# Performance work log

Hardware: AMD Instinct MI355X
Metric: run time of the kernel (lower is better)

The kernel has to match this reference:

```python
import jax, jax.numpy as jnp
import numpy as np

HIDDEN = 1024


def setup_inputs() -> dict:
    key = jax.random.key(0)
    ks = jax.random.split(key, 8)
    x_in, y_in, out_dim, hidden = 1024, 1024, 1024, HIDDEN
    Nx, Ny = 4096, 4096
    s = lambda d: 1.0 / np.sqrt(d)
    return {
        "x": jax.random.normal(ks[0], (Nx, x_in), jnp.float32),
        "y": jax.random.normal(ks[1], (Ny, y_in), jnp.float32),
        "Wq": jax.random.normal(ks[2], (hidden, x_in), jnp.float32) * s(x_in),
        "bq": jnp.zeros((hidden,), jnp.float32),
        "Wk": jax.random.normal(ks[3], (hidden, y_in), jnp.float32) * s(y_in),
        "bk": jnp.zeros((hidden,), jnp.float32),
        "Wv": jax.random.normal(ks[4], (out_dim, y_in), jnp.float32) * s(y_in),
        "bv": jnp.zeros((out_dim,), jnp.float32),
    }


def reference(x, y, Wq, bq, Wk, bk, Wv, bv):
    # Linear projections (torch Linear: x @ W.T + b)
    q = x @ Wq.T + bq          # [Nx, H]
    k = y @ Wk.T + bk          # [Ny, H]
    v = y @ Wv.T + bv          # [Ny, D_out]
    scores = (q @ k.T) / jnp.sqrt(jnp.asarray(HIDDEN, q.dtype))  # [Nx, Ny]
    attn = jax.nn.softmax(scores, axis=1)
    return attn @ v            # [Nx, D_out]
```

## Files before the change

kernel.cpp:

```cpp
#include <hip/hip_runtime.h>
#include <cstdint>
#include <cstddef>

typedef __attribute__((ext_vector_type(8))) __bf16 bf16x8;
typedef __attribute__((ext_vector_type(4))) float  f32x4;

#define WAITCNT_VM(n)   ((n & 0xF) | 0x70 | 0xF00 | (((n) >> 4) << 14))
#define WAITCNT_LGKM(n) (0xF | 0x70 | ((n) << 8) | (3 << 14))

__device__ __forceinline__ unsigned short f32_to_bf16(float f) {
    union { float f; unsigned int u; } cv;
    cv.f = f;
    unsigned int u = cv.u;
    return (unsigned short)((u + 0x7fffu + ((u >> 16) & 1u)) >> 16);
}

__device__ __forceinline__ float bf16_to_f32(unsigned short h) {
    union { unsigned int u; float f; } cv;
    cv.u = ((unsigned int)h) << 16;
    return cv.f;
}

__device__ __forceinline__ void async_copy16(const unsigned short* g, unsigned short* lds) {
    __builtin_amdgcn_global_load_lds(
        (const __attribute__((address_space(1))) unsigned int*)g,
        (__attribute__((address_space(3))) unsigned int*)lds,
        16, 0, 0);
}

__global__ __launch_bounds__(256) void cast_all(
    const float* __restrict__ x,  const float* __restrict__ y,
    const float* __restrict__ wq, const float* __restrict__ wk, const float* __restrict__ wv,
    unsigned short* __restrict__ xb,  unsigned short* __restrict__ yb,
    unsigned short* __restrict__ wqb, unsigned short* __restrict__ wkb,
    unsigned short* __restrict__ wvb, float* __restrict__ lsum)
{
    int b = blockIdx.x;
    if (b >= 11264) {
        float4 z = {0.f, 0.f, 0.f, 0.f};
#pragma unroll
        for (int t = 0; t < 4; ++t)
            ((float4*)lsum)[threadIdx.x * 4 + t] = z;
        return;
    }
    const float* s; unsigned short* d; int base;
    if      (b < 4096)  { s = x;  d = xb;  base = b; }
    else if (b < 8192)  { s = y;  d = yb;  base = b - 4096; }
    else if (b < 9216)  { s = wq; d = wqb; base = b - 8192; }
    else if (b < 10240) { s = wk; d = wkb; base = b - 9216; }
    else                { s = wv; d = wvb; base = b - 10240; }
    int i = base * 256 + threadIdx.x;
    float4 v = ((const float4*)s)[i];
    ushort4 o;
    o.x = f32_to_bf16(v.x);
    o.y = f32_to_bf16(v.y);
    o.z = f32_to_bf16(v.z);
    o.w = f32_to_bf16(v.w);
    ((ushort4*)d)[i] = o;
}

__device__ __forceinline__ void gemm_core_pf(
    const unsigned short* __restrict__ A, const unsigned short* __restrict__ B,
    int K, int rowBase, int colBase, int kBeg, int kEnd,
    unsigned short* ldsA, unsigned short* ldsB, f32x4 acc[4][4])
{
    const int tid  = threadIdx.x;
    const int lane = tid & 63;
    const int wave = tid >> 6;
    const int quad = lane >> 4;
    const int r    = lane & 15;
    const int wm   = wave >> 1;
    const int wn   = wave & 1;

    const int c1 = tid + 256;
    const long aOff0 = (long)(rowBase + (tid >> 2)) * K + (tid & 3) * 8;
    const long aOff1 = (long)(rowBase + (c1  >> 2)) * K + (c1  & 3) * 8;
    const long bOff0 = (long)(colBase + (tid >> 2)) * K + (tid & 3) * 8;
    const long bOff1 = (long)(colBase + (c1  >> 2)) * K + (c1  & 3) * 8;
    unsigned short* ldsA0 = ldsA + tid * 8;
    unsigned short* ldsA1 = ldsA + c1 * 8;
    unsigned short* ldsB0 = ldsB + tid * 8;
    unsigned short* ldsB1 = ldsB + c1 * 8;

    const int aReadOff = (wm * 64 + r) * 32 + quad * 8;
    const int bReadOff = (wn * 64 + r) * 32 + quad * 8;

    const int nSteps = (kEnd - kBeg) >> 5;

    async_copy16(A + aOff0 + kBeg, ldsA0);
    async_copy16(A + aOff1 + kBeg, ldsA1);
    async_copy16(B + bOff0 + kBeg, ldsB0);
    async_copy16(B + bOff1 + kBeg, ldsB1);

    for (int s = 0; s < nSteps; ++s) {
        const int cur = (s & 1) << 12;
        const int nxt = cur ^ 4096;
        __builtin_amdgcn_s_waitcnt(0);
        __syncthreads();
        if (s + 1 < nSteps) {
            const int kn = kBeg + ((s + 1) << 5);
            async_copy16(A + aOff0 + kn, ldsA0 + nxt);
            async_copy16(A + aOff1 + kn, ldsA1 + nxt);
            async_copy16(B + bOff0 + kn, ldsB0 + nxt);
            async_copy16(B + bOff1 + kn, ldsB1 + nxt);
        }
        bf16x8 af[4], bfr[4];
#pragma unroll
        for (int i = 0; i < 4; ++i)
            af[i] = *(const bf16x8*)(ldsA + cur + aReadOff + i * 16 * 32);
#pragma unroll
        for (int j = 0; j < 4; ++j)
            bfr[j] = *(const bf16x8*)(ldsB + cur + bReadOff + j * 16 * 32);
#pragma unroll
        for (int i = 0; i < 4; ++i)
#pragma unroll
            for (int j = 0; j < 4; ++j)
                acc[i][j] = __builtin_amdgcn_mfma_f32_16x16x32_bf16(af[i], bfr[j], acc[i][j], 0, 0, 0);
    }
}

__global__ __launch_bounds__(256, 2)
void proj_batched(const unsigned short* __restrict__ xb, const unsigned short* __restrict__ yb,
                  const unsigned short* __restrict__ wqb, const unsigned short* __restrict__ wkb,
                  const unsigned short* __restrict__ wvb,
                  unsigned short* __restrict__ q, unsigned short* __restrict__ k,
                  unsigned short* __restrict__ vt,
                  const float* __restrict__ bq, const float* __restrict__ bk,
                  const float* __restrict__ bv)
{
    __shared__ __align__(16) unsigned short ldsA[2 * 128 * 32];
    __shared__ __align__(16) unsigned short ldsB[2 * 128 * 32];

    const int b = blockIdx.x;
    const int z = b >> 8;
    const int rb = b & 255;

    const unsigned short *A, *B;
    unsigned short* C;
    const float* bias;
    int N, rowBase, colBase;
    bool biasPerRow;
    if (z == 0) {
        A = xb; B = wqb; C = q; bias = bq; N = 1024; biasPerRow = false;
        colBase = (rb >> 5) * 128; rowBase = (rb & 31) * 128;
    } else if (z == 1) {
        A = yb; B = wkb; C = k; bias = bk; N = 1024; biasPerRow = false;
        colBase = (rb >> 5) * 128; rowBase = (rb & 31) * 128;
    } else {
        A = wvb; B = yb; C = vt; bias = bv; N = 4096; biasPerRow = true;
        colBase = (rb >> 3) * 128; rowBase = (rb & 7) * 128;
    }

    f32x4 acc[4][4];
#pragma unroll
    for (int i = 0; i < 4; ++i)
#pragma unroll
        for (int j = 0; j < 4; ++j)
            acc[i][j] = (f32x4){0.f, 0.f, 0.f, 0.f};

    gemm_core_pf(A, B, 1024, rowBase, colBase, 0, 1024, ldsA, ldsB, acc);

    const int lane = threadIdx.x & 63;
    const int wave = threadIdx.x >> 6;
    const int quad = lane >> 4;
    const int r    = lane & 15;
    const int orow0 = rowBase + (wave >> 1) * 64 + quad * 4;
    const int ocol0 = colBase + (wave & 1) * 64 + r;

#pragma unroll
    for (int i = 0; i < 4; ++i)
#pragma unroll
        for (int e = 0; e < 4; ++e) {
            const int row = orow0 + i * 16 + e;
            const float brow = biasPerRow ? bias[row] : 0.f;
#pragma unroll
            for (int j = 0; j < 4; ++j) {
                const int col = ocol0 + j * 16;
                const float bb = biasPerRow ? brow : bias[col];
                C[(long)row * N + col] = f32_to_bf16(acc[i][j][e] + bb);
            }
        }
}

__device__ __forceinline__ void stage_half(const unsigned short* src, long rstep,
                                           unsigned short* ldsLane) {
    async_copy16(src, ldsLane);
    async_copy16(src + rstep, ldsLane + 4096);
}

__device__ __forceinline__ void gemm256_core(
    const unsigned short* __restrict__ A, const unsigned short* __restrict__ B,
    int K, int rowBase, int colBase, int kBeg, int nTiles,
    unsigned short* lds, f32x4 acc[8][4])
{
    const int tid  = threadIdx.x;
    const int lane = tid & 63;
    const int wid  = tid >> 6;
    const int quad = lane >> 4;
    const int r    = lane & 15;
    const int wm   = wid >> 2;
    const int wn   = wid & 3;

    const int row0 = tid >> 3;
    const int chs8 = (((tid & 7) ^ (row0 & 7)) << 3);
    const unsigned short* As = A + (long)(rowBase + row0) * K + chs8 + kBeg;
    const unsigned short* Bs = B + (long)(colBase + row0) * K + chs8 + kBeg;
    const long rstep = (long)K * 64;
    const long hstep = (long)K * 128;
    unsigned short* ldsLane = lds + tid * 8;

    const int aRd = (wm << 13) + (r << 6);
    const int bRd = 16384 + (wn << 12) + (r << 6);
    const int sw0 = ((quad ^ (r & 7)) << 3);
    const int sw1 = (((quad + 4) ^ (r & 7)) << 3);

    stage_half(As,         rstep, ldsLane);
    stage_half(As + hstep, rstep, ldsLane + 8192);
    stage_half(Bs,         rstep, ldsLane + 16384);
    stage_half(Bs + hstep, rstep, ldsLane + 24576);
    if (nTiles > 1) {
        stage_half(Bs + 64,         rstep, ldsLane + 32768 + 16384);
        stage_half(Bs + hstep + 64, rstep, ldsLane + 32768 + 24576);
    }
    __builtin_amdgcn_s_waitcnt(WAITCNT_VM(4));
    __builtin_amdgcn_s_barrier();
    __builtin_amdgcn_sched_barrier(0);

    bf16x8 aE[4], aO[4], bX[4], bY[4];
#pragma unroll
    for (int i = 0; i < 4; ++i)
        aE[i] = *(const bf16x8*)(lds + aRd + i * 1024 + sw0);
#pragma unroll
    for (int j = 0; j < 4; ++j)
        bX[j] = *(const bf16x8*)(lds + bRd + j * 1024 + sw0);

    for (int T = 0; T < nTiles; ++T) {
        const int cur = (T & 1) << 15;
        const int nxt = cur ^ 32768;

#pragma unroll
        for (int i = 0; i < 4; ++i)
            aO[i] = *(const bf16x8*)(lds + cur + aRd + (4 + i) * 1024 + sw0);
        __builtin_amdgcn_s_waitcnt(WAITCNT_LGKM(4));
        __builtin_amdgcn_sched_barrier(0);
        __builtin_amdgcn_s_setprio(1);
#pragma unroll
        for (int i = 0; i < 4; ++i)
#pragma unroll
            for (int j = 0; j < 4; ++j)
                acc[i][j] = __builtin_amdgcn_mfma_f32_16x16x32_bf16(aE[i], bX[j], acc[i][j], 0, 0, 0);
        __builtin_amdgcn_s_setprio(0);
        __builtin_amdgcn_sched_barrier(0);
        __builtin_amdgcn_s_barrier();
        if (T + 1 < nTiles) stage_half(As + (T + 1) * 64, rstep, ldsLane + nxt);

#pragma unroll
        for (int i = 0; i < 4; ++i)
            aE[i] = *(const bf16x8*)(lds + cur + aRd + i * 1024 + sw1);
#pragma unroll
        for (int j = 0; j < 4; ++j)
            bY[j] = *(const bf16x8*)(lds + cur + bRd + j * 1024 + sw1);
        __builtin_amdgcn_s_waitcnt(WAITCNT_LGKM(8));
        __builtin_amdgcn_sched_barrier(0);
        __builtin_amdgcn_s_setprio(1);
#pragma unroll
        for (int i = 0; i < 4; ++i)
#pragma unroll
            for (int j = 0; j < 4; ++j)
                acc[4 + i][j] = __builtin_amdgcn_mfma_f32_16x16x32_bf16(aO[i], bX[j], acc[4 + i][j], 0, 0, 0);
        __builtin_amdgcn_s_setprio(0);
        __builtin_amdgcn_sched_barrier(0);
        __builtin_amdgcn_s_barrier();
        if (T + 1 < nTiles) stage_half(As + hstep + (T + 1) * 64, rstep, ldsLane + nxt + 8192);

#pragma unroll
        for (int i = 0; i < 4; ++i)
            aO[i] = *(const bf16x8*)(lds + cur + aRd + (4 + i) * 1024 + sw1);
        __builtin_amdgcn_s_waitcnt(WAITCNT_LGKM(4));
        __builtin_amdgcn_sched_barrier(0);
        __builtin_amdgcn_s_setprio(1);
#pragma unroll
        for (int i = 0; i < 4; ++i)
#pragma unroll
            for (int j = 0; j < 4; ++j)
                acc[i][j] = __builtin_amdgcn_mfma_f32_16x16x32_bf16(aE[i], bY[j], acc[i][j], 0, 0, 0);
        __builtin_amdgcn_s_setprio(0);
        __builtin_amdgcn_sched_barrier(0);
        __builtin_amdgcn_s_barrier();
        if (T + 2 < nTiles) stage_half(Bs + (T + 2) * 64, rstep, ldsLane + cur + 16384);

        if (T + 1 < nTiles) {
            if (T + 2 < nTiles) __builtin_amdgcn_s_waitcnt(WAITCNT_VM(2));
            else                __builtin_amdgcn_s_waitcnt(WAITCNT_VM(0));
            __builtin_amdgcn_s_barrier();
            __builtin_amdgcn_sched_barrier(0);
#pragma unroll
            for (int i = 0; i < 4; ++i)
                aE[i] = *(const bf16x8*)(lds + nxt + aRd + i * 1024 + sw0);
#pragma unroll
            for (int j = 0; j < 4; ++j)
                bX[j] = *(const bf16x8*)(lds + nxt + bRd + j * 1024 + sw0);
            __builtin_amdgcn_s_waitcnt(WAITCNT_LGKM(8));
        } else {
            __builtin_amdgcn_s_waitcnt(WAITCNT_LGKM(0));
        }
        __builtin_amdgcn_sched_barrier(0);
        __builtin_amdgcn_s_setprio(1);
#pragma unroll
        for (int i = 0; i < 4; ++i)
#pragma unroll
            for (int j = 0; j < 4; ++j)
                acc[4 + i][j] = __builtin_amdgcn_mfma_f32_16x16x32_bf16(aO[i], bY[j], acc[4 + i][j], 0, 0, 0);
        __builtin_amdgcn_s_setprio(0);
        __builtin_amdgcn_sched_barrier(0);
        if (T + 2 < nTiles) stage_half(Bs + hstep + (T + 2) * 64, rstep, ldsLane + cur + 24576);
    }
}

__global__ __launch_bounds__(512, 2)
void scores_gemm256(const unsigned short* __restrict__ q, const unsigned short* __restrict__ k,
                    unsigned short* __restrict__ P, float* __restrict__ lsum, float scale2)
{
    __shared__ __align__(16) unsigned short lds[2 * 32768];

    const int bid = blockIdx.x;
    const int swz = (bid & 7) * 32 + (bid >> 3);
    const int mt = swz >> 4, nt = swz & 15;
    const int rowBase = mt * 256;
    const int colBase = nt * 256;

    f32x4 acc[8][4];
#pragma unroll
    for (int i = 0; i < 8; ++i)
#pragma unroll
        for (int j = 0; j < 4; ++j)
            acc[i][j] = (f32x4){0.f, 0.f, 0.f, 0.f};

    gemm256_core(q, k, 1024, rowBase, colBase, 0, 16, lds, acc);

    const int lane = threadIdx.x & 63;
    const int wid  = threadIdx.x >> 6;
    const int quad = lane >> 4;
    const int r    = lane & 15;
    const int orow0 = rowBase + (wid >> 2) * 128 + quad * 4;
    const int ocol0 = colBase + (wid & 3) * 64 + r;

#pragma unroll
    for (int mi = 0; mi < 8; ++mi)
#pragma unroll
        for (int e = 0; e < 4; ++e) {
            const int row = orow0 + mi * 16 + e;
            float rs = 0.f;
#pragma unroll
            for (int nj = 0; nj < 4; ++nj) {
                const float p = exp2f(acc[mi][nj][e] * scale2);
                rs += p;
                P[(long)row * 4096 + ocol0 + nj * 16] = f32_to_bf16(p);
            }
#pragma unroll
            for (int m = 1; m < 16; m <<= 1) rs += __shfl_xor(rs, m, 64);
            if (r == 0) atomicAdd(&lsum[row], rs);
        }
}

template <int ATOMIC>
__global__ __launch_bounds__(512, 2)
void out_gemm256(const unsigned short* __restrict__ P, const unsigned short* __restrict__ vt,
                 void* __restrict__ Out)
{
    __shared__ __align__(16) unsigned short lds[2 * 32768];

    const int bid = blockIdx.x;
    const int swz = (bid & 7) * 32 + (bid >> 3);
    const int z  = swz & 3;
    const int nt = (swz >> 2) & 3;
    const int mt = swz >> 4;
    const int rowBase = mt * 256;
    const int colBase = nt * 256;
    const int kBeg = z * 1024;

    f32x4 acc[8][4];
#pragma unroll
    for (int i = 0; i < 8; ++i)
#pragma unroll
        for (int j = 0; j < 4; ++j)
            acc[i][j] = (f32x4){0.f, 0.f, 0.f, 0.f};

    gemm256_core(P, vt, 4096, rowBase, colBase, kBeg, 16, lds, acc);

    const int lane = threadIdx.x & 63;
    const int wid  = threadIdx.x >> 6;
    const int quad = lane >> 4;
    const int r    = lane & 15;
    const int orow0 = rowBase + (wid >> 2) * 128 + quad * 4;
    const int ocol0 = colBase + (wid & 3) * 64 + r;

#pragma unroll
    for (int mi = 0; mi < 8; ++mi)
#pragma unroll
        for (int e = 0; e < 4; ++e) {
            const int row = orow0 + mi * 16 + e;
#pragma unroll
            for (int nj = 0; nj < 4; ++nj) {
                const int col = ocol0 + nj * 16;
                if (ATOMIC) {
                    atomicAdd(&((float*)Out)[(long)row * 1024 + col], acc[mi][nj][e]);
                } else {
                    unsigned short* parts = (unsigned short*)Out + (size_t)z * (4096 * 1024);
                    parts[(long)row * 1024 + col] = f32_to_bf16(acc[mi][nj][e]);
                }
            }
        }
}

__global__ __launch_bounds__(256) void reduce_norm4(const unsigned short* __restrict__ parts,
                                                    const float* __restrict__ lsum,
                                                    float* __restrict__ O) {
    const int i = blockIdx.x * 256 + threadIdx.x;
    const float inv = 1.0f / lsum[i >> 8];
    const size_t stride = (size_t)(4096 * 1024) / 4;
    ushort4 a = ((const ushort4*)parts)[i];
    ushort4 b = ((const ushort4*)parts)[i + stride];
    ushort4 c = ((const ushort4*)parts)[i + 2 * stride];
    ushort4 d = ((const ushort4*)parts)[i + 3 * stride];
    float4 o;
    o.x = (bf16_to_f32(a.x) + bf16_to_f32(b.x) + bf16_to_f32(c.x) + bf16_to_f32(d.x)) * inv;
    o.y = (bf16_to_f32(a.y) + bf16_to_f32(b.y) + bf16_to_f32(c.y) + bf16_to_f32(d.y)) * inv;
    o.z = (bf16_to_f32(a.z) + bf16_to_f32(b.z) + bf16_to_f32(c.z) + bf16_to_f32(d.z)) * inv;
    o.w = (bf16_to_f32(a.w) + bf16_to_f32(b.w) + bf16_to_f32(c.w) + bf16_to_f32(d.w)) * inv;
    ((float4*)O)[i] = o;
}

__global__ __launch_bounds__(256) void norm_rows(float* __restrict__ O, const float* __restrict__ lsum) {
    int i = blockIdx.x * 256 + threadIdx.x;
    const float inv = 1.0f / lsum[i >> 8];
    float4 v = ((const float4*)O)[i];
    v.x *= inv; v.y *= inv; v.z *= inv; v.w *= inv;
    ((float4*)O)[i] = v;
}

extern "C" void kernel_launch(void* const* d_in, const int* in_sizes, int n_in,
                              void* d_out, int out_size, void* d_ws, size_t ws_size,
                              hipStream_t stream) {
    const float* x  = (const float*)d_in[0];
    const float* y  = (const float*)d_in[1];
    const float* Wq = (const float*)d_in[2];
    const float* bq = (const float*)d_in[3];
    const float* Wk = (const float*)d_in[4];
    const float* bk = (const float*)d_in[5];
    const float* Wv = (const float*)d_in[6];
    const float* bv = (const float*)d_in[7];

    constexpr int Nx = 4096, Ny = 4096, H = 1024, Dv = 1024, Kin = 1024;

    char* ws = (char*)d_ws;
    size_t off = 0;
    auto carve = [&](size_t bytes) {
        char* p = ws + off;
        off += (bytes + 255) & ~(size_t)255;
        return p;
    };

    unsigned short* q_bf  = (unsigned short*)carve((size_t)Nx * H * 2);
    unsigned short* k_bf  = (unsigned short*)carve((size_t)Ny * H * 2);
    unsigned short* vt_bf = (unsigned short*)carve((size_t)Dv * Ny * 2);
    float*          lsum  = (float*)carve((size_t)Nx * sizeof(float));

    char* overlay = ws + off;
    unsigned short* x_bf  = (unsigned short*)overlay;
    unsigned short* y_bf  = x_bf  + (size_t)Nx * Kin;
    unsigned short* Wq_bf = y_bf  + (size_t)Ny * Kin;
    unsigned short* Wk_bf = Wq_bf + (size_t)H  * Kin;
    unsigned short* Wv_bf = Wk_bf + (size_t)H  * Kin;
    unsigned short* P_bf  = (unsigned short*)overlay;

    const size_t overlay_bytes = (size_t)Nx * Ny * 2;
    const size_t partsBytes = (size_t)Nx * Dv * 2;
    unsigned short* parts = (unsigned short*)(overlay + overlay_bytes);
    const size_t need_parts = (size_t)((overlay + overlay_bytes + 4 * partsBytes) - ws);
    const bool useParts = ws_size >= need_parts;

    if (!useParts)
        hipMemsetAsync(d_out, 0, (size_t)Nx * Dv * sizeof(float), stream);

    cast_all<<<11265, 256, 0, stream>>>(x, y, Wq, Wk, Wv, x_bf, y_bf, Wq_bf, Wk_bf, Wv_bf, lsum);

    proj_batched<<<768, 256, 0, stream>>>(x_bf, y_bf, Wq_bf, Wk_bf, Wv_bf,
                                          q_bf, k_bf, vt_bf, bq, bk, bv);

    const float scale2 = 1.4426950408889634f / 32.0f;
    scores_gemm256<<<256, 512, 0, stream>>>(q_bf, k_bf, P_bf, lsum, scale2);

    if (useParts) {
        out_gemm256<0><<<256, 512, 0, stream>>>(P_bf, vt_bf, parts);
        reduce_norm4<<<(Nx * Dv / 4) / 256, 256, 0, stream>>>(parts, lsum, (float*)d_out);
    } else {
        out_gemm256<1><<<256, 512, 0, stream>>>(P_bf, vt_bf, d_out);
        norm_rows<<<Nx * Dv / 4 / 256, 256, 0, stream>>>((float*)d_out, lsum);
    }
}
```

Baseline: 223.1 us.

## Fuse all attention stages into one cooperative persistent kernel with grid syncs

Replaces the five separate launches (cast, projection, scores, output GEMM, reduce) with a single cooperative kernel of 256 blocks that runs each stage in turn, separated by grid-wide syncs. It also moves the projection GEMM onto the 256x256 latency-tuned GEMM core, so only 192 blocks are active in that stage. The aim is to remove launch gaps and tail effects between kernels. In exchange, the cast and reduce stages run as grid-stride loops on fewer threads, the projection stage leaves some blocks idle, and grid syncs add overhead.

```diff
diff --git a/kernel.cpp b/kernel.cpp
--- a/kernel.cpp
+++ b/kernel.cpp
@@ -1,6 +1,9 @@
 #include <hip/hip_runtime.h>
+#include <hip/hip_cooperative_groups.h>
 #include <cstdint>
 #include <cstddef>
+
+namespace cg = cooperative_groups;
 
 typedef __attribute__((ext_vector_type(8))) __bf16 bf16x8;
 typedef __attribute__((ext_vector_type(4))) float  f32x4;
@@ -26,6 +29,324 @@
         (const __attribute__((address_space(1))) unsigned int*)g,
         (__attribute__((address_space(3))) unsigned int*)lds,
         16, 0, 0);
+}
+
+#define G256_BAR  __builtin_amdgcn_s_barrier()
+#define G256_SB   __builtin_amdgcn_sched_barrier(0)
+#define G256_PR1  __builtin_amdgcn_s_setprio(1)
+#define G256_PR0  __builtin_amdgcn_s_setprio(0)
+
+__device__ __forceinline__ void gemm256_la(
+    const unsigned short* __restrict__ A, const unsigned short* __restrict__ B,
+    int K, int rowBase, int colBase, int kBeg, int nTiles,
+    unsigned short* lds, f32x4 acc[8][4])
+{
+    const int tid  = threadIdx.x;
+    const int lane = tid & 63;
+    const int wid  = tid >> 6;
+    const int quad = lane >> 4;
+    const int r    = lane & 15;
+    const int wm   = wid >> 2;
+    const int wn   = wid & 3;
+
+    const int row0 = tid >> 3;
+    const int chs8 = (((tid & 7) ^ (row0 & 7)) << 3);
+    const unsigned short* As = A + (long)(rowBase + row0) * K + chs8 + kBeg;
+    const unsigned short* Bs = B + (long)(colBase + row0) * K + chs8 + kBeg;
+    const long rstep = (long)K * 64;
+    const long hstep = (long)K * 128;
+    unsigned short* ldsLane = lds + tid * 8;
+
+    const int aRd = (wm << 13) + (r << 6);
+    const int bRd = 16384 + (wn << 12) + (r << 6);
+    const int sw0 = ((quad ^ (r & 7)) << 3);
+    const int sw1 = (((quad + 4) ^ (r & 7)) << 3);
+
+    auto STG = [&](const unsigned short* src, int ldsOff) {
+        async_copy16(src,         ldsLane + ldsOff);
+        async_copy16(src + rstep, ldsLane + ldsOff + 4096);
+    };
+
+    STG(As,         0);
+    STG(As + hstep, 8192);
+    STG(Bs,         16384);
+    STG(Bs + hstep, 24576);
+    if (nTiles > 1) {
+        STG(Bs + 64,         32768 + 16384);
+        STG(Bs + hstep + 64, 32768 + 24576);
+    }
+    __builtin_amdgcn_s_waitcnt(WAITCNT_VM(4));
+    G256_BAR;
+    G256_SB;
+
+    bf16x8 aE[4], aO[4], bX[4], bY[4];
+#pragma unroll
+    for (int i = 0; i < 4; ++i)
+        aE[i] = *(const bf16x8*)(lds + aRd + i * 1024 + sw0);
+#pragma unroll
+    for (int j = 0; j < 4; ++j)
+        bX[j] = *(const bf16x8*)(lds + bRd + j * 1024 + sw0);
+
+    for (int T = 0; T < nTiles; ++T) {
+        const int cur = (T & 1) << 15;
+        const int nxt = cur ^ 32768;
+
+#pragma unroll
+        for (int i = 0; i < 4; ++i)
+            aO[i] = *(const bf16x8*)(lds + cur + aRd + (4 + i) * 1024 + sw0);
+        __builtin_amdgcn_s_waitcnt(WAITCNT_LGKM(4));
+        G256_SB;
+        G256_PR1;
+#pragma unroll
+        for (int i = 0; i < 4; ++i)
+#pragma unroll
+            for (int j = 0; j < 4; ++j)
+                acc[i][j] = __builtin_amdgcn_mfma_f32_16x16x32_bf16(aE[i], bX[j], acc[i][j], 0, 0, 0);
+        G256_PR0;
+        G256_SB;
+        G256_BAR;
+        if (T + 1 < nTiles) STG(As + (T + 1) * 64, nxt);
+
+#pragma unroll
+        for (int i = 0; i < 4; ++i)
+            aE[i] = *(const bf16x8*)(lds + cur + aRd + i * 1024 + sw1);
+#pragma unroll
+        for (int j = 0; j < 4; ++j)
+            bY[j] = *(const bf16x8*)(lds + cur + bRd + j * 1024 + sw1);
+        __builtin_amdgcn_s_waitcnt(WAITCNT_LGKM(8));
+        G256_SB;
+        G256_PR1;
+#pragma unroll
+        for (int i = 0; i < 4; ++i)
+#pragma unroll
+            for (int j = 0; j < 4; ++j)
+                acc[4 + i][j] = __builtin_amdgcn_mfma_f32_16x16x32_bf16(aO[i], bX[j], acc[4 + i][j], 0, 0, 0);
+        G256_PR0;
+        G256_SB;
+        G256_BAR;
+        if (T + 1 < nTiles) STG(As + hstep + (T + 1) * 64, nxt + 8192);
+
+#pragma unroll
+        for (int i = 0; i < 4; ++i)
+            aO[i] = *(const bf16x8*)(lds + cur + aRd + (4 + i) * 1024 + sw1);
+        __builtin_amdgcn_s_waitcnt(WAITCNT_LGKM(4));
+        G256_SB;
+        G256_PR1;
+#pragma unroll
+        for (int i = 0; i < 4; ++i)
+#pragma unroll
+            for (int j = 0; j < 4; ++j)
+                acc[i][j] = __builtin_amdgcn_mfma_f32_16x16x32_bf16(aE[i], bY[j], acc[i][j], 0, 0, 0);
+        G256_PR0;
+        G256_SB;
+        G256_BAR;
+        if (T + 2 < nTiles) STG(Bs + (T + 2) * 64, cur + 16384);
+
+        if (T + 1 < nTiles) {
+            if (T + 2 < nTiles) __builtin_amdgcn_s_waitcnt(WAITCNT_VM(2));
+            else                __builtin_amdgcn_s_waitcnt(WAITCNT_VM(0));
+            G256_BAR;
+            G256_SB;
+#pragma unroll
+            for (int i = 0; i < 4; ++i)
+                aE[i] = *(const bf16x8*)(lds + nxt + aRd + i * 1024 + sw0);
+#pragma unroll
+            for (int j = 0; j < 4; ++j)
+                bX[j] = *(const bf16x8*)(lds + nxt + bRd + j * 1024 + sw0);
+            __builtin_amdgcn_s_waitcnt(WAITCNT_LGKM(8));
+        } else {
+            __builtin_amdgcn_s_waitcnt(WAITCNT_LGKM(0));
+        }
+        G256_SB;
+        G256_PR1;
+#pragma unroll
+        for (int i = 0; i < 4; ++i)
+#pragma unroll
+            for (int j = 0; j < 4; ++j)
+                acc[4 + i][j] = __builtin_amdgcn_mfma_f32_16x16x32_bf16(aO[i], bY[j], acc[4 + i][j], 0, 0, 0);
+        G256_PR0;
+        G256_SB;
+        if (T + 2 < nTiles) STG(Bs + hstep + (T + 2) * 64, cur + 24576);
+    }
+}
+
+__global__ __launch_bounds__(512, 2)
+void mega(const float* __restrict__ x,  const float* __restrict__ y,
+          const float* __restrict__ wq, const float* __restrict__ wk, const float* __restrict__ wv,
+          const float* __restrict__ bq, const float* __restrict__ bk, const float* __restrict__ bv,
+          unsigned short* __restrict__ xb,  unsigned short* __restrict__ yb,
+          unsigned short* __restrict__ wqb, unsigned short* __restrict__ wkb,
+          unsigned short* __restrict__ wvb,
+          unsigned short* __restrict__ q, unsigned short* __restrict__ k,
+          unsigned short* __restrict__ vt, unsigned short* __restrict__ P,
+          unsigned short* __restrict__ parts, float* __restrict__ lsum,
+          float* __restrict__ O, float scale2)
+{
+    __shared__ __align__(16) unsigned short lds[2 * 32768];
+    cg::grid_group gg = cg::this_grid();
+
+    const int tid  = threadIdx.x;
+    const int bid  = blockIdx.x;
+    const long gtid = (long)bid * 512 + tid;
+
+    {
+        float4 z4 = {0.f, 0.f, 0.f, 0.f};
+        for (long u = gtid; u < 2884608L; u += 131072L) {
+            if (u < 1024) { ((float4*)lsum)[u] = z4; continue; }
+            long v = u - 1024;
+            const float* s; unsigned short* d; long idx;
+            if      (v < 1048576L) { s = x;  d = xb;  idx = v; }
+            else if (v < 2097152L) { s = y;  d = yb;  idx = v - 1048576L; }
+            else if (v < 2359296L) { s = wq; d = wqb; idx = v - 2097152L; }
+            else if (v < 2621440L) { s = wk; d = wkb; idx = v - 2359296L; }
+            else                   { s = wv; d = wvb; idx = v - 2621440L; }
+            float4 vv = ((const float4*)s)[idx];
+            ushort4 o;
+            o.x = f32_to_bf16(vv.x);
+            o.y = f32_to_bf16(vv.y);
+            o.z = f32_to_bf16(vv.z);
+            o.w = f32_to_bf16(vv.w);
+            ((ushort4*)d)[idx] = o;
+        }
+    }
+    gg.sync();
+
+    const int lane = tid & 63;
+    const int wid  = tid >> 6;
+    const int quad = lane >> 4;
+    const int rr   = lane & 15;
+
+    if (bid < 192) {
+        const int z  = bid >> 6;
+        const int rb = bid & 63;
+        const unsigned short *A, *B;
+        unsigned short* C;
+        const float* bias;
+        int Nout, rowBase, colBase;
+        bool perRow;
+        if (z == 0) {
+            A = xb; B = wqb; C = q; bias = bq; Nout = 1024; perRow = false;
+            rowBase = (rb >> 2) * 256; colBase = (rb & 3) * 256;
+        } else if (z == 1) {
+            A = yb; B = wkb; C = k; bias = bk; Nout = 1024; perRow = false;
+            rowBase = (rb >> 2) * 256; colBase = (rb & 3) * 256;
+        } else {
+            A = wvb; B = yb; C = vt; bias = bv; Nout = 4096; perRow = true;
+            rowBase = (rb >> 4) * 256; colBase = (rb & 15) * 256;
+        }
+
+        f32x4 acc[8][4];
+#pragma unroll
+        for (int i = 0; i < 8; ++i)
+#pragma unroll
+            for (int j = 0; j < 4; ++j)
+                acc[i][j] = (f32x4){0.f, 0.f, 0.f, 0.f};
+
+        gemm256_la(A, B, 1024, rowBase, colBase, 0, 16, lds, acc);
+
+        const int orow0 = rowBase + (wid >> 2) * 128 + quad * 4;
+        const int ocol0 = colBase + (wid & 3) * 64 + rr;
+#pragma unroll
+        for (int mi = 0; mi < 8; ++mi)
+#pragma unroll
+            for (int e = 0; e < 4; ++e) {
+                const int row = orow0 + mi * 16 + e;
+                const float brow = perRow ? bias[row] : 0.f;
+#pragma unroll
+                for (int nj = 0; nj < 4; ++nj) {
+                    const int col = ocol0 + nj * 16;
+                    const float bb = perRow ? brow : bias[col];
+                    C[(long)row * Nout + col] = f32_to_bf16(acc[mi][nj][e] + bb);
+                }
+            }
+    }
+    gg.sync();
+
+    {
+        const int swz = (bid & 7) * 32 + (bid >> 3);
+        const int mt = swz >> 4, nt = swz & 15;
+        const int rowBase = mt * 256;
+        const int colBase = nt * 256;
+
+        f32x4 acc[8][4];
+#pragma unroll
+        for (int i = 0; i < 8; ++i)
+#pragma unroll
+            for (int j = 0; j < 4; ++j)
+                acc[i][j] = (f32x4){0.f, 0.f, 0.f, 0.f};
+
+        gemm256_la(q, k, 1024, rowBase, colBase, 0, 16, lds, acc);
+
+        const int orow0 = rowBase + (wid >> 2) * 128 + quad * 4;
+        const int ocol0 = colBase + (wid & 3) * 64 + rr;
+#pragma unroll
+        for (int mi = 0; mi < 8; ++mi)
+#pragma unroll
+            for (int e = 0; e < 4; ++e) {
+                const int row = orow0 + mi * 16 + e;
+                float rs = 0.f;
+#pragma unroll
+                for (int nj = 0; nj < 4; ++nj) {
+                    const float p = exp2f(acc[mi][nj][e] * scale2);
+                    rs += p;
+                    P[(long)row * 4096 + ocol0 + nj * 16] = f32_to_bf16(p);
+                }
+#pragma unroll
+                for (int m = 1; m < 16; m <<= 1) rs += __shfl_xor(rs, m, 64);
+                if (rr == 0) atomicAdd(&lsum[row], rs);
+            }
+    }
+    gg.sync();
+
+    {
+        const int swz = (bid & 7) * 32 + (bid >> 3);
+        const int z  = swz & 3;
+        const int nt = (swz >> 2) & 3;
+        const int mt = swz >> 4;
+        const int rowBase = mt * 256;
+        const int colBase = nt * 256;
+        const int kBeg = z * 1024;
+
+        f32x4 acc[8][4];
+#pragma unroll
+        for (int i = 0; i < 8; ++i)
+#pragma unroll
+            for (int j = 0; j < 4; ++j)
+                acc[i][j] = (f32x4){0.f, 0.f, 0.f, 0.f};
+
+        gemm256_la(P, vt, 4096, rowBase, colBase, kBeg, 16, lds, acc);
+
+        unsigned short* part = parts + (size_t)z * (4096 * 1024);
+        const int orow0 = rowBase + (wid >> 2) * 128 + quad * 4;
+        const int ocol0 = colBase + (wid & 3) * 64 + rr;
+#pragma unroll
+        for (int mi = 0; mi < 8; ++mi)
+#pragma unroll
+            for (int e = 0; e < 4; ++e) {
+                const int row = orow0 + mi * 16 + e;
+#pragma unroll
+                for (int nj = 0; nj < 4; ++nj)
+                    part[(long)row * 1024 + ocol0 + nj * 16] = f32_to_bf16(acc[mi][nj][e]);
+            }
+    }
+    gg.sync();
+
+    {
+        const size_t stride = 1048576;
+        for (long i = gtid; i < 1048576L; i += 131072L) {
+            const float inv = 1.0f / lsum[i >> 8];
+            ushort4 a = ((const ushort4*)parts)[i];
+            ushort4 b = ((const ushort4*)parts)[i + stride];
+            ushort4 c = ((const ushort4*)parts)[i + 2 * stride];
+            ushort4 d = ((const ushort4*)parts)[i + 3 * stride];
+            float4 o;
+            o.x = (bf16_to_f32(a.x) + bf16_to_f32(b.x) + bf16_to_f32(c.x) + bf16_to_f32(d.x)) * inv;
+            o.y = (bf16_to_f32(a.y) + bf16_to_f32(b.y) + bf16_to_f32(c.y) + bf16_to_f32(d.y)) * inv;
+            o.z = (bf16_to_f32(a.z) + bf16_to_f32(b.z) + bf16_to_f32(c.z) + bf16_to_f32(d.z)) * inv;
+            o.w = (bf16_to_f32(a.w) + bf16_to_f32(b.w) + bf16_to_f32(c.w) + bf16_to_f32(d.w)) * inv;
+            ((float4*)O)[i] = o;
+        }
+    }
 }
 
 __global__ __launch_bounds__(256) void cast_all(
@@ -59,262 +380,58 @@
     ((ushort4*)d)[i] = o;
 }
 
-__device__ __forceinline__ void gemm_core_pf(
-    const unsigned short* __restrict__ A, const unsigned short* __restrict__ B,
-    int K, int rowBase, int colBase, int kBeg, int kEnd,
-    unsigned short* ldsA, unsigned short* ldsB, f32x4 acc[4][4])
+__global__ __launch_bounds__(512, 2)
+void proj256(const unsigned short* __restrict__ xb, const unsigned short* __restrict__ yb,
+             const unsigned short* __restrict__ wqb, const unsigned short* __restrict__ wkb,
+             const unsigned short* __restrict__ wvb,
+             unsigned short* __restrict__ q, unsigned short* __restrict__ k,
+             unsigned short* __restrict__ vt,
+             const float* __restrict__ bq, const float* __restrict__ bk,
+             const float* __restrict__ bv)
 {
-    const int tid  = threadIdx.x;
-    const int lane = tid & 63;
-    const int wave = tid >> 6;
-    const int quad = lane >> 4;
-    const int r    = lane & 15;
-    const int wm   = wave >> 1;
-    const int wn   = wave & 1;
-
-    const int c1 = tid + 256;
-    const long aOff0 = (long)(rowBase + (tid >> 2)) * K + (tid & 3) * 8;
-    const long aOff1 = (long)(rowBase + (c1  >> 2)) * K + (c1  & 3) * 8;
-    const long bOff0 = (long)(colBase + (tid >> 2)) * K + (tid & 3) * 8;
-    const long bOff1 = (long)(colBase + (c1  >> 2)) * K + (c1  & 3) * 8;
-    unsigned short* ldsA0 = ldsA + tid * 8;
-    unsigned short* ldsA1 = ldsA + c1 * 8;
-    unsigned short* ldsB0 = ldsB + tid * 8;
-    unsigned short* ldsB1 = ldsB + c1 * 8;
-
-    const int aReadOff = (wm * 64 + r) * 32 + quad * 8;
-    const int bReadOff = (wn * 64 + r) * 32 + quad * 8;
-
-    const int nSteps = (kEnd - kBeg) >> 5;
-
-    async_copy16(A + aOff0 + kBeg, ldsA0);
-    async_copy16(A + aOff1 + kBeg, ldsA1);
-    async_copy16(B + bOff0 + kBeg, ldsB0);
-    async_copy16(B + bOff1 + kBeg, ldsB1);
-
-    for (int s = 0; s < nSteps; ++s) {
-        const int cur = (s & 1) << 12;
-        const int nxt = cur ^ 4096;
-        __builtin_amdgcn_s_waitcnt(0);
-        __syncthreads();
-        if (s + 1 < nSteps) {
-            const int kn = kBeg + ((s + 1) << 5);
-            async_copy16(A + aOff0 + kn, ldsA0 + nxt);
-            async_copy16(A + aOff1 + kn, ldsA1 + nxt);
-            async_copy16(B + bOff0 + kn, ldsB0 + nxt);
-            async_copy16(B + bOff1 + kn, ldsB1 + nxt);
-        }
-        bf16x8 af[4], bfr[4];
-#pragma unroll
-        for (int i = 0; i < 4; ++i)
-            af[i] = *(const bf16x8*)(ldsA + cur + aReadOff + i * 16 * 32);
-#pragma unroll
-        for (int j = 0; j < 4; ++j)
-            bfr[j] = *(const bf16x8*)(ldsB + cur + bReadOff + j * 16 * 32);
-#pragma unroll
-        for (int i = 0; i < 4; ++i)
-#pragma unroll
-            for (int j = 0; j < 4; ++j)
-                acc[i][j] = __builtin_amdgcn_mfma_f32_16x16x32_bf16(af[i], bfr[j], acc[i][j], 0, 0, 0);
-    }
-}
-
-__global__ __launch_bounds__(256, 2)
-void proj_batched(const unsigned short* __restrict__ xb, const unsigned short* __restrict__ yb,
-                  const unsigned short* __restrict__ wqb, const unsigned short* __restrict__ wkb,
-                  const unsigned short* __restrict__ wvb,
-                  unsigned short* __restrict__ q, unsigned short* __restrict__ k,
-                  unsigned short* __restrict__ vt,
-                  const float* __restrict__ bq, const float* __restrict__ bk,
-                  const float* __restrict__ bv)
-{
-    __shared__ __align__(16) unsigned short ldsA[2 * 128 * 32];
-    __shared__ __align__(16) unsigned short ldsB[2 * 128 * 32];
-
-    const int b = blockIdx.x;
-    const int z = b >> 8;
-    const int rb = b & 255;
-
+    __shared__ __align__(16) unsigned short lds[2 * 32768];
+    const int bid = blockIdx.x;
+    const int z  = bid >> 6;
+    const int rb = bid & 63;
     const unsigned short *A, *B;
     unsigned short* C;
     const float* bias;
-    int N, rowBase, colBase;
-    bool biasPerRow;
+    int Nout, rowBase, colBase;
+    bool perRow;
     if (z == 0) {
-        A = xb; B = wqb; C = q; bias = bq; N = 1024; biasPerRow = false;
-        colBase = (rb >> 5) * 128; rowBase = (rb & 31) * 128;
+        A = xb; B = wqb; C = q; bias = bq; Nout = 1024; perRow = false;
+        rowBase = (rb >> 2) * 256; colBase = (rb & 3) * 256;
     } else if (z == 1) {
-        A = yb; B = wkb; C = k; bias = bk; N = 1024; biasPerRow = false;
-        colBase = (rb >> 5) * 128; rowBase = (rb & 31) * 128;
+        A = yb; B = wkb; C = k; bias = bk; Nout = 1024; perRow = false;
+        rowBase = (rb >> 2) * 256; colBase = (rb & 3) * 256;
     } else {
-        A = wvb; B = yb; C = vt; bias = bv; N = 4096; biasPerRow = true;
-        colBase = (rb >> 3) * 128; rowBase = (rb & 7) * 128;
-    }
-
-    f32x4 acc[4][4];
-#pragma unroll
-    for (int i = 0; i < 4; ++i)
+        A = wvb; B = yb; C = vt; bias = bv; Nout = 4096; perRow = true;
+        rowBase = (rb >> 4) * 256; colBase = (rb & 15) * 256;
+    }
+    f32x4 acc[8][4];
+#pragma unroll
+    for (int i = 0; i < 8; ++i)
 #pragma unroll
         for (int j = 0; j < 4; ++j)
             acc[i][j] = (f32x4){0.f, 0.f, 0.f, 0.f};
-
-    gemm_core_pf(A, B, 1024, rowBase, colBase, 0, 1024, ldsA, ldsB, acc);
-
+    gemm256_la(A, B, 1024, rowBase, colBase, 0, 16, lds, acc);
     const int lane = threadIdx.x & 63;
-    const int wave = threadIdx.x >> 6;
-    const int quad = lane >> 4;
-    const int r    = lane & 15;
-    const int orow0 = rowBase + (wave >> 1) * 64 + quad * 4;
-    const int ocol0 = colBase + (wave & 1) * 64 + r;
-
-#pragma unroll
-    for (int i = 0; i < 4; ++i)
+    const int wid  = threadIdx.x >> 6;
+    const int orow0 = rowBase + (wid >> 2) * 128 + (lane >> 4) * 4;
+    const int ocol0 = colBase + (wid & 3) * 64 + (lane & 15);
+#pragma unroll
+    for (int mi = 0; mi < 8; ++mi)
 #pragma unroll
         for (int e = 0; e < 4; ++e) {
-            const int row = orow0 + i * 16 + e;
-            const float brow = biasPerRow ? bias[row] : 0.f;
-#pragma unroll
-            for (int j = 0; j < 4; ++j) {
-                const int col = ocol0 + j * 16;
-                const float bb = biasPerRow ? brow : bias[col];
-                C[(long)row * N + col] = f32_to_bf16(acc[i][j][e] + bb);
+            const int row = orow0 + mi * 16 + e;
+            const float brow = perRow ? bias[row] : 0.f;
+#pragma unroll
+            for (int nj = 0; nj < 4; ++nj) {
+                const int col = ocol0 + nj * 16;
+                const float bb = perRow ? brow : bias[col];
+                C[(long)row * Nout + col] = f32_to_bf16(acc[mi][nj][e] + bb);
             }
         }
-}
-
-__device__ __forceinline__ void stage_half(const unsigned short* src, long rstep,
-                                           unsigned short* ldsLane) {
-    async_copy16(src, ldsLane);
-    async_copy16(src + rstep, ldsLane + 4096);
-}
-
-__device__ __forceinline__ void gemm256_core(
-    const unsigned short* __restrict__ A, const unsigned short* __restrict__ B,
-    int K, int rowBase, int colBase, int kBeg, int nTiles,
-    unsigned short* lds, f32x4 acc[8][4])
-{
-    const int tid  = threadIdx.x;
-    const int lane = tid & 63;
-    const int wid  = tid >> 6;
-    const int quad = lane >> 4;
-    const int r    = lane & 15;
-    const int wm   = wid >> 2;
-    const int wn   = wid & 3;
-
-    const int row0 = tid >> 3;
-    const int chs8 = (((tid & 7) ^ (row0 & 7)) << 3);
-    const unsigned short* As = A + (long)(rowBase + row0) * K + chs8 + kBeg;
-    const unsigned short* Bs = B + (long)(colBase + row0) * K + chs8 + kBeg;
-    const long rstep = (long)K * 64;
-    const long hstep = (long)K * 128;
-    unsigned short* ldsLane = lds + tid * 8;
-
-    const int aRd = (wm << 13) + (r << 6);
-    const int bRd = 16384 + (wn << 12) + (r << 6);
-    const int sw0 = ((quad ^ (r & 7)) << 3);
-    const int sw1 = (((quad + 4) ^ (r & 7)) << 3);
-
-    stage_half(As,         rstep, ldsLane);
-    stage_half(As + hstep, rstep, ldsLane + 8192);
-    stage_half(Bs,         rstep, ldsLane + 16384);
-    stage_half(Bs + hstep, rstep, ldsLane + 24576);
-    if (nTiles > 1) {
-        stage_half(Bs + 64,         rstep, ldsLane + 32768 + 16384);
-        stage_half(Bs + hstep + 64, rstep, ldsLane + 32768 + 24576);
-    }
-    __builtin_amdgcn_s_waitcnt(WAITCNT_VM(4));
-    __builtin_amdgcn_s_barrier();
-    __builtin_amdgcn_sched_barrier(0);
-
-    bf16x8 aE[4], aO[4], bX[4], bY[4];
-#pragma unroll
-    for (int i = 0; i < 4; ++i)
-        aE[i] = *(const bf16x8*)(lds + aRd + i * 1024 + sw0);
-#pragma unroll
-    for (int j = 0; j < 4; ++j)
-        bX[j] = *(const bf16x8*)(lds + bRd + j * 1024 + sw0);
-
-    for (int T = 0; T < nTiles; ++T) {
-        const int cur = (T & 1) << 15;
-        const int nxt = cur ^ 32768;
-
-#pragma unroll
-        for (int i = 0; i < 4; ++i)
-            aO[i] = *(const bf16x8*)(lds + cur + aRd + (4 + i) * 1024 + sw0);
-        __builtin_amdgcn_s_waitcnt(WAITCNT_LGKM(4));
-        __builtin_amdgcn_sched_barrier(0);
-        __builtin_amdgcn_s_setprio(1);
-#pragma unroll
-        for (int i = 0; i < 4; ++i)
-#pragma unroll
-            for (int j = 0; j < 4; ++j)
-                acc[i][j] = __builtin_amdgcn_mfma_f32_16x16x32_bf16(aE[i], bX[j], acc[i][j], 0, 0, 0);
-        __builtin_amdgcn_s_setprio(0);
-        __builtin_amdgcn_sched_barrier(0);
-        __builtin_amdgcn_s_barrier();
-        if (T + 1 < nTiles) stage_half(As + (T + 1) * 64, rstep, ldsLane + nxt);
-
-#pragma unroll
-        for (int i = 0; i < 4; ++i)
-            aE[i] = *(const bf16x8*)(lds + cur + aRd + i * 1024 + sw1);
-#pragma unroll
-        for (int j = 0; j < 4; ++j)
-            bY[j] = *(const bf16x8*)(lds + cur + bRd + j * 1024 + sw1);
-        __builtin_amdgcn_s_waitcnt(WAITCNT_LGKM(8));
-        __builtin_amdgcn_sched_barrier(0);
-        __builtin_amdgcn_s_setprio(1);
-#pragma unroll
-        for (int i = 0; i < 4; ++i)
-#pragma unroll
-            for (int j = 0; j < 4; ++j)
-                acc[4 + i][j] = __builtin_amdgcn_mfma_f32_16x16x32_bf16(aO[i], bX[j], acc[4 + i][j], 0, 0, 0);
-        __builtin_amdgcn_s_setprio(0);
-        __builtin_amdgcn_sched_barrier(0);
-        __builtin_amdgcn_s_barrier();
-        if (T + 1 < nTiles) stage_half(As + hstep + (T + 1) * 64, rstep, ldsLane + nxt + 8192);
-
-#pragma unroll
-        for (int i = 0; i < 4; ++i)
-            aO[i] = *(const bf16x8*)(lds + cur + aRd + (4 + i) * 1024 + sw1);
-        __builtin_amdgcn_s_waitcnt(WAITCNT_LGKM(4));
-        __builtin_amdgcn_sched_barrier(0);
-        __builtin_amdgcn_s_setprio(1);
-#pragma unroll
-        for (int i = 0; i < 4; ++i)
-#pragma unroll
-            for (int j = 0; j < 4; ++j)
-                acc[i][j] = __builtin_amdgcn_mfma_f32_16x16x32_bf16(aE[i], bY[j], acc[i][j], 0, 0, 0);
-        __builtin_amdgcn_s_setprio(0);
-        __builtin_amdgcn_sched_barrier(0);
-        __builtin_amdgcn_s_barrier();
-        if (T + 2 < nTiles) stage_half(Bs + (T + 2) * 64, rstep, ldsLane + cur + 16384);
-
-        if (T + 1 < nTiles) {
-            if (T + 2 < nTiles) __builtin_amdgcn_s_waitcnt(WAITCNT_VM(2));
-            else                __builtin_amdgcn_s_waitcnt(WAITCNT_VM(0));
-            __builtin_amdgcn_s_barrier();
-            __builtin_amdgcn_sched_barrier(0);
-#pragma unroll
-            for (int i = 0; i < 4; ++i)
-                aE[i] = *(const bf16x8*)(lds + nxt + aRd + i * 1024 + sw0);
-#pragma unroll
-            for (int j = 0; j < 4; ++j)
-                bX[j] = *(const bf16x8*)(lds + nxt + bRd + j * 1024 + sw0);
-            __builtin_amdgcn_s_waitcnt(WAITCNT_LGKM(8));
-        } else {
-            __builtin_amdgcn_s_waitcnt(WAITCNT_LGKM(0));
-        }
-        __builtin_amdgcn_sched_barrier(0);
-        __builtin_amdgcn_s_setprio(1);
-#pragma unroll
-        for (int i = 0; i < 4; ++i)
-#pragma unroll
-            for (int j = 0; j < 4; ++j)
-                acc[4 + i][j] = __builtin_amdgcn_mfma_f32_16x16x32_bf16(aO[i], bY[j], acc[4 + i][j], 0, 0, 0);
-        __builtin_amdgcn_s_setprio(0);
-        __builtin_amdgcn_sched_barrier(0);
-        if (T + 2 < nTiles) stage_half(Bs + hstep + (T + 2) * 64, rstep, ldsLane + cur + 24576);
-    }
 }
 
 __global__ __launch_bounds__(512, 2)
@@ -322,29 +439,22 @@
                     unsigned short* __restrict__ P, float* __restrict__ lsum, float scale2)
 {
     __shared__ __align__(16) unsigned short lds[2 * 32768];
-
     const int bid = blockIdx.x;
     const int swz = (bid & 7) * 32 + (bid >> 3);
     const int mt = swz >> 4, nt = swz & 15;
     const int rowBase = mt * 256;
     const int colBase = nt * 256;
-
     f32x4 acc[8][4];
 #pragma unroll
     for (int i = 0; i < 8; ++i)
 #pragma unroll
         for (int j = 0; j < 4; ++j)
             acc[i][j] = (f32x4){0.f, 0.f, 0.f, 0.f};
-
-    gemm256_core(q, k, 1024, rowBase, colBase, 0, 16, lds, acc);
-
+    gemm256_la(q, k, 1024, rowBase, colBase, 0, 16, lds, acc);
     const int lane = threadIdx.x & 63;
     const int wid  = threadIdx.x >> 6;
-    const int quad = lane >> 4;
-    const int r    = lane & 15;
-    const int orow0 = rowBase + (wid >> 2) * 128 + quad * 4;
-    const int ocol0 = colBase + (wid & 3) * 64 + r;
-
+    const int orow0 = rowBase + (wid >> 2) * 128 + (lane >> 4) * 4;
+    const int ocol0 = colBase + (wid & 3) * 64 + (lane & 15);
 #pragma unroll
     for (int mi = 0; mi < 8; ++mi)
 #pragma unroll
@@ -359,17 +469,15 @@
             }
 #pragma unroll
             for (int m = 1; m < 16; m <<= 1) rs += __shfl_xor(rs, m, 64);
-            if (r == 0) atomicAdd(&lsum[row], rs);
-        }
-}
-
-template <int ATOMIC>
+            if ((lane & 15) == 0) atomicAdd(&lsum[row], rs);
+        }
+}
+
 __global__ __launch_bounds__(512, 2)
-void out_gemm256(const unsigned short* __restrict__ P, const unsigned short* __restrict__ vt,
-                 void* __restrict__ Out)
+void out_gemm256_atomic(const unsigned short* __restrict__ P, const unsigned short* __restrict__ vt,
+                        float* __restrict__ Out)
 {
     __shared__ __align__(16) unsigned short lds[2 * 32768];
-
     const int bid = blockIdx.x;
     const int swz = (bid & 7) * 32 + (bid >> 3);
     const int z  = swz & 3;
@@ -377,58 +485,26 @@
     const int mt = swz >> 4;
     const int rowBase = mt * 256;
     const int colBase = nt * 256;
-    const int kBeg = z * 1024;
-
     f32x4 acc[8][4];
 #pragma unroll
     for (int i = 0; i < 8; ++i)
 #pragma unroll
         for (int j = 0; j < 4; ++j)
             acc[i][j] = (f32x4){0.f, 0.f, 0.f, 0.f};
-
-    gemm256_core(P, vt, 4096, rowBase, colBase, kBeg, 16, lds, acc);
-
+    gemm256_la(P, vt, 4096, rowBase, colBase, z * 1024, 16, lds, acc);
     const int lane = threadIdx.x & 63;
     const int wid  = threadIdx.x >> 6;
-    const int quad = lane >> 4;
-    const int r    = lane & 15;
-    const int orow0 = rowBase + (wid >> 2) * 128 + quad * 4;
-    const int ocol0 = colBase + (wid & 3) * 64 + r;
-
+    const int orow0 = rowBase + (wid >> 2) * 128 + (lane >> 4) * 4;
+    const int ocol0 = colBase + (wid & 3) * 64 + (lane & 15);
 #pragma unroll
     for (int mi = 0; mi < 8; ++mi)
 #pragma unroll
         for (int e = 0; e < 4; ++e) {
             const int row = orow0 + mi * 16 + e;
 #pragma unroll
-            for (int nj = 0; nj < 4; ++nj) {
-                const int col = ocol0 + nj * 16;
-                if (ATOMIC) {
-                    atomicAdd(&((float*)Out)[(long)row * 1024 + col], acc[mi][nj][e]);
-                } else {
-                    unsigned short* parts = (unsigned short*)Out + (size_t)z * (4096 * 1024);
-                    parts[(long)row * 1024 + col] = f32_to_bf16(acc[mi][nj][e]);
-                }
-            }
-        }
-}
-
-__global__ __launch_bounds__(256) void reduce_norm4(const unsigned short* __restrict__ parts,
-                                                    const float* __restrict__ lsum,
-                                                    float* __restrict__ O) {
-    const int i = blockIdx.x * 256 + threadIdx.x;
-    const float inv = 1.0f / lsum[i >> 8];
-    const size_t stride = (size_t)(4096 * 1024) / 4;
-    ushort4 a = ((const ushort4*)parts)[i];
-    ushort4 b = ((const ushort4*)parts)[i + stride];
-    ushort4 c = ((const ushort4*)parts)[i + 2 * stride];
-    ushort4 d = ((const ushort4*)parts)[i + 3 * stride];
-    float4 o;
-    o.x = (bf16_to_f32(a.x) + bf16_to_f32(b.x) + bf16_to_f32(c.x) + bf16_to_f32(d.x)) * inv;
-    o.y = (bf16_to_f32(a.y) + bf16_to_f32(b.y) + bf16_to_f32(c.y) + bf16_to_f32(d.y)) * inv;
-    o.z = (bf16_to_f32(a.z) + bf16_to_f32(b.z) + bf16_to_f32(c.z) + bf16_to_f32(d.z)) * inv;
-    o.w = (bf16_to_f32(a.w) + bf16_to_f32(b.w) + bf16_to_f32(c.w) + bf16_to_f32(d.w)) * inv;
-    ((float4*)O)[i] = o;
+            for (int nj = 0; nj < 4; ++nj)
+                atomicAdd(&Out[(long)row * 1024 + ocol0 + nj * 16], acc[mi][nj][e]);
+        }
 }
 
 __global__ __launch_bounds__(256) void norm_rows(float* __restrict__ O, const float* __restrict__ lsum) {
@@ -480,22 +556,26 @@
     const size_t need_parts = (size_t)((overlay + overlay_bytes + 4 * partsBytes) - ws);
     const bool useParts = ws_size >= need_parts;
 
-    if (!useParts)
-        hipMemsetAsync(d_out, 0, (size_t)Nx * Dv * sizeof(float), stream);
-
-    cast_all<<<11265, 256, 0, stream>>>(x, y, Wq, Wk, Wv, x_bf, y_bf, Wq_bf, Wk_bf, Wv_bf, lsum);
-
-    proj_batched<<<768, 256, 0, stream>>>(x_bf, y_bf, Wq_bf, Wk_bf, Wv_bf,
-                                          q_bf, k_bf, vt_bf, bq, bk, bv);
-
-    const float scale2 = 1.4426950408889634f / 32.0f;
-    scores_gemm256<<<256, 512, 0, stream>>>(q_bf, k_bf, P_bf, lsum, scale2);
+    float scale2 = 1.4426950408889634f / 32.0f;
+    float* outF = (float*)d_out;
 
     if (useParts) {
-        out_gemm256<0><<<256, 512, 0, stream>>>(P_bf, vt_bf, parts);
-        reduce_norm4<<<(Nx * Dv / 4) / 256, 256, 0, stream>>>(parts, lsum, (float*)d_out);
+        void* args[] = {
+            (void*)&x, (void*)&y, (void*)&Wq, (void*)&Wk, (void*)&Wv,
+            (void*)&bq, (void*)&bk, (void*)&bv,
+            (void*)&x_bf, (void*)&y_bf, (void*)&Wq_bf, (void*)&Wk_bf, (void*)&Wv_bf,
+            (void*)&q_bf, (void*)&k_bf, (void*)&vt_bf, (void*)&P_bf,
+            (void*)&parts, (void*)&lsum, (void*)&outF, (void*)&scale2
+        };
+        (void)hipLaunchCooperativeKernel(reinterpret_cast<void*>(mega),
+                                         dim3(256), dim3(512), args, 0, stream);
     } else {
-        out_gemm256<1><<<256, 512, 0, stream>>>(P_bf, vt_bf, d_out);
-        norm_rows<<<Nx * Dv / 4 / 256, 256, 0, stream>>>((float*)d_out, lsum);
-    }
-}
+        (void)hipMemsetAsync(d_out, 0, (size_t)Nx * Dv * sizeof(float), stream);
+        cast_all<<<11265, 256, 0, stream>>>(x, y, Wq, Wk, Wv, x_bf, y_bf, Wq_bf, Wk_bf, Wv_bf, lsum);
+        proj256<<<192, 512, 0, stream>>>(x_bf, y_bf, Wq_bf, Wk_bf, Wv_bf,
+                                         q_bf, k_bf, vt_bf, bq, bk, bv);
+        scores_gemm256<<<256, 512, 0, stream>>>(q_bf, k_bf, P_bf, lsum, scale2);
+        out_gemm256_atomic<<<256, 512, 0, stream>>>(P_bf, vt_bf, outF);
+        norm_rows<<<Nx * Dv / 4 / 256, 256, 0, stream>>>(outF, lsum);
+    }
+}
```

Result: slower. 398.9 us (+78.8%).
